# Kernel tuning notes

Hardware: AMD Instinct MI355X
Metric: run time of the kernel (lower is better)

## Reference

```python
import jax, jax.numpy as jnp
import numpy as np

B, S, D, U = 32, 2048, 512, 512

def setup_inputs() -> dict:
    key = jax.random.key(0)
    k1, k2, k3, k4, k5 = jax.random.split(key, 5)
    passage = jax.random.normal(k1, (B, S, D), dtype=jnp.float32)
    hidden = jax.random.normal(k2, (B, D), dtype=jnp.float32)
    mask = jnp.ones((B, S), dtype=jnp.float32)
    # learned params (Dense kernels, glorot-ish scale)
    W1 = jax.random.normal(k3, (D, U), dtype=jnp.float32) / np.sqrt(D)
    W2 = jax.random.normal(k4, (D, U), dtype=jnp.float32) / np.sqrt(D)
    Vw = jax.random.normal(k5, (U, 1), dtype=jnp.float32) / np.sqrt(U)
    Vb = jnp.zeros((1,), dtype=jnp.float32)
    return {"passage": passage, "hidden": hidden, "mask": mask,
            "W1": W1, "W2": W2, "Vw": Vw, "Vb": Vb}

def reference(passage, hidden, mask, W1, W2, Vw, Vb):
    # passage: [B,S,D], hidden: [B,D], mask: [B,S]
    h_proj = jnp.einsum('bd,du->bu', hidden, W2)[:, None, :]        # [B,1,U]
    p_proj = jnp.einsum('bsd,du->bsu', passage, W1)                  # [B,S,U]
    score = jnp.einsum('bsu,uo->bso', jnp.tanh(p_proj + h_proj), Vw) + Vb  # [B,S,1]
    score = score + ((1.0 - mask) * -1e30)[:, :, None]
    attention_weights = jax.nn.softmax(score, axis=1)                # [B,S,1]
    context_vector = jnp.sum(attention_weights * passage, axis=1)    # [B,D]
    return context_vector, attention_weights
```

## Files before the change

### kernel.cpp

```cpp
#include <hip/hip_runtime.h>
#include <hip/hip_bf16.h>
#include <cstddef>


#define NB 32
#define NS 2048
#define ND 512
#define NU 512

typedef __bf16 bf16_t;
typedef __bf16 bf16x8 __attribute__((ext_vector_type(8)));
typedef float floatx4 __attribute__((ext_vector_type(4)));

__global__ __launch_bounds__(256) void prep_kernel(
    const float* __restrict__ W1, bf16_t* __restrict__ W1p,
    const float* __restrict__ hidden, const float* __restrict__ W2,
    float* __restrict__ hproj) {
    if (blockIdx.x < 128) {
        int wave = threadIdx.x >> 6, lane = threadIdx.x & 63;
        int f = (blockIdx.x << 2) + wave;
        int kc = f >> 5, ng = f & 31;
        int q = lane >> 4, c = lane & 15;
        const float* src = W1 + (kc * 32 + q * 8) * 512 + ng * 16 + c;
        bf16x8 w;
#pragma unroll
        for (int jj = 0; jj < 8; ++jj) w[jj] = (bf16_t)src[jj * 512];
        ((bf16x8*)W1p)[(f << 6) + lane] = w;
    } else {
        __shared__ float h[ND];
        __shared__ float part[256];
        int bi = blockIdx.x - 128;
        int b = bi >> 2, ug = bi & 3;
        int t = threadIdx.x;
        h[t] = hidden[b * ND + t];
        h[t + 256] = hidden[b * ND + t + 256];
        __syncthreads();
        int u = (ug << 7) + (t & 127);
        int d0 = (t >> 7) << 8;
        float acc = 0.f;
#pragma unroll 8
        for (int d = d0; d < d0 + 256; ++d) acc = fmaf(h[d], W2[d * NU + u], acc);
        part[t] = acc;
        __syncthreads();
        if (t < 128) hproj[b * NU + u] = part[t] + part[t + 128];
    }
}

__global__ __launch_bounds__(512, 4) void score_kernel(
    const float* __restrict__ passage, const bf16_t* __restrict__ W1p,
    const float* __restrict__ hproj, const float* __restrict__ Vw,
    const float* __restrict__ Vb, float* __restrict__ scores) {
    __shared__ bf16_t Asf[64 * 512];
    const int tid = threadIdx.x;
    const int wave = tid >> 6, lane = tid & 63;
    const int q = lane >> 4, c = lane & 15;
    const int m0 = blockIdx.x * 64;
    const int b = m0 >> 11;
    const int ng0 = wave << 2;
    const bf16x8* Wq = (const bf16x8*)W1p;

#define LOAD_B(dst, kc_) {                                                   \
    _Pragma("unroll")                                                        \
    for (int j = 0; j < 4; ++j)                                              \
        dst[j] = Wq[((((kc_) << 5) + ng0 + j) << 6) + lane]; }

    bf16x8 b0[4], b1[4];
    LOAD_B(b0, 0);
    LOAD_B(b1, 1);

#pragma unroll
    for (int it = 0; it < 8; ++it) {
        int idx = it * 512 + tid;
        int row = idx >> 6, c8 = idx & 63;
        const float4* src = (const float4*)(passage + ((size_t)(m0 + row) << 9)) + (c8 << 1);
        float4 v0 = src[0], v1 = src[1];
        bf16x8 w;
        w[0] = (bf16_t)v0.x; w[1] = (bf16_t)v0.y; w[2] = (bf16_t)v0.z; w[3] = (bf16_t)v0.w;
        w[4] = (bf16_t)v1.x; w[5] = (bf16_t)v1.y; w[6] = (bf16_t)v1.z; w[7] = (bf16_t)v1.w;
        ((bf16x8*)(Asf + (row << 9)))[c8 ^ (row & 7)] = w;
    }
    __syncthreads();

    floatx4 acc[4][4];
#pragma unroll
    for (int i = 0; i < 4; ++i)
#pragma unroll
        for (int j = 0; j < 4; ++j) { floatx4 z = {0.f, 0.f, 0.f, 0.f}; acc[i][j] = z; }

#pragma unroll
    for (int kc = 0; kc < 16; ++kc) {
        bf16x8 bn[4];
        if (kc < 14) LOAD_B(bn, kc + 2);
        bf16x8 a[4];
        int chunk = (kc << 2) + q;
#pragma unroll
        for (int i = 0; i < 4; ++i)
            a[i] = ((const bf16x8*)(Asf + ((i * 16 + c) << 9)))[chunk ^ (c & 7)];
#pragma unroll
        for (int j = 0; j < 4; ++j)
#pragma unroll
            for (int i = 0; i < 4; ++i)
                acc[i][j] = __builtin_amdgcn_mfma_f32_16x16x32_bf16(a[i], b0[j], acc[i][j], 0, 0, 0);
#pragma unroll
        for (int j = 0; j < 4; ++j) { b0[j] = b1[j]; b1[j] = bn[j]; }
    }
#undef LOAD_B

    float sp[4][4];
#pragma unroll
    for (int i = 0; i < 4; ++i)
#pragma unroll
        for (int r = 0; r < 4; ++r) sp[i][r] = 0.f;
#pragma unroll
    for (int j = 0; j < 4; ++j) {
        int n = (wave << 6) + (j << 4) + c;
        float hp = hproj[(b << 9) + n];
        float vw = Vw[n];
#pragma unroll
        for (int i = 0; i < 4; ++i)
#pragma unroll
            for (int r = 0; r < 4; ++r) {
                float x = acc[i][j][r] + hp;
                float e = __expf(2.0f * x);
                float t = 1.0f - 2.0f * __builtin_amdgcn_rcpf(e + 1.0f);
                sp[i][r] = fmaf(t, vw, sp[i][r]);
            }
    }
#pragma unroll
    for (int off = 1; off < 16; off <<= 1)
#pragma unroll
        for (int i = 0; i < 4; ++i)
#pragma unroll
            for (int r = 0; r < 4; ++r)
                sp[i][r] += __shfl_xor(sp[i][r], off, 64);

    __syncthreads();
    float* red = (float*)Asf;
    if (c == 0) {
#pragma unroll
        for (int i = 0; i < 4; ++i)
#pragma unroll
            for (int r = 0; r < 4; ++r)
                red[wave * 64 + i * 16 + q * 4 + r] = sp[i][r];
    }
    __syncthreads();
    if (tid < 64) {
        float s = Vb[0];
#pragma unroll
        for (int w = 0; w < 8; ++w) s += red[w * 64 + tid];
        scores[m0 + tid] = s;
    }
}

__global__ __launch_bounds__(1024) void softmax_kernel(
    const float* __restrict__ mask, float* __restrict__ attn) {
    __shared__ float smx[16], ssm[16];
    int b = blockIdx.x, tid = threadIdx.x;
    int wave = tid >> 6, lane = tid & 63;
    const int base = b * NS;
    float v0 = attn[base + tid] + (1.0f - mask[base + tid]) * (-1e30f);
    float v1 = attn[base + 1024 + tid] + (1.0f - mask[base + 1024 + tid]) * (-1e30f);
    float mx = fmaxf(v0, v1);
#pragma unroll
    for (int off = 1; off < 64; off <<= 1) mx = fmaxf(mx, __shfl_xor(mx, off, 64));
    if (lane == 0) smx[wave] = mx;
    __syncthreads();
    mx = smx[0];
#pragma unroll
    for (int w = 1; w < 16; ++w) mx = fmaxf(mx, smx[w]);
    v0 = __expf(v0 - mx); v1 = __expf(v1 - mx);
    float sum = v0 + v1;
#pragma unroll
    for (int off = 1; off < 64; off <<= 1) sum += __shfl_xor(sum, off, 64);
    if (lane == 0) ssm[wave] = sum;
    __syncthreads();
    sum = 0.f;
#pragma unroll
    for (int w = 0; w < 16; ++w) sum += ssm[w];
    float inv = 1.0f / sum;
    attn[base + tid] = v0 * inv;
    attn[base + 1024 + tid] = v1 * inv;
}

__global__ __launch_bounds__(512) void context_kernel(
    const float* __restrict__ passage, const float* __restrict__ attn,
    float* __restrict__ ctx) {
    __shared__ float4 part[512];
    int bb = blockIdx.x >> 5, sc = blockIdx.x & 31, t = threadIdx.x;
    int col = t & 127, qh = t >> 7;
    const float4* p = (const float4*)(passage + (((size_t)bb * NS + sc * 64 + qh * 16) << 9));
    const float* wp = attn + bb * NS + sc * 64 + qh * 16;
    float ax = 0.f, ay = 0.f, az = 0.f, aw = 0.f;
#pragma unroll 16
    for (int s = 0; s < 16; ++s) {
        float w = wp[s];
        float4 v = p[(size_t)s * 128 + col];
        ax = fmaf(w, v.x, ax); ay = fmaf(w, v.y, ay);
        az = fmaf(w, v.z, az); aw = fmaf(w, v.w, aw);
    }
    float4 mine; mine.x = ax; mine.y = ay; mine.z = az; mine.w = aw;
    part[t] = mine;
    __syncthreads();
    if (t < 128) {
        float4 o1 = part[t + 128], o2 = part[t + 256], o3 = part[t + 384];
        float* dst = ctx + bb * ND + t * 4;
        atomicAdd(dst + 0, ax + o1.x + o2.x + o3.x);
        atomicAdd(dst + 1, ay + o1.y + o2.y + o3.y);
        atomicAdd(dst + 2, az + o1.z + o2.z + o3.z);
        atomicAdd(dst + 3, aw + o1.w + o2.w + o3.w);
    }
}

extern "C" void kernel_launch(void* const* d_in, const int* in_sizes, int n_in,
                              void* d_out, int out_size, void* d_ws, size_t ws_size,
                              hipStream_t stream) {
    const float* passage = (const float*)d_in[0];
    const float* hidden  = (const float*)d_in[1];
    const float* mask    = (const float*)d_in[2];
    const float* W1      = (const float*)d_in[3];
    const float* W2      = (const float*)d_in[4];
    const float* Vw      = (const float*)d_in[5];
    const float* Vb      = (const float*)d_in[6];

    float* ctx  = (float*)d_out;
    float* attn = (float*)d_out + NB * ND;

    bf16_t* W1p  = (bf16_t*)d_ws;
    float* hproj = (float*)((char*)d_ws + (size_t)NU * ND * 2);

    hipMemsetAsync(ctx, 0, (size_t)NB * ND * sizeof(float), stream);
    prep_kernel<<<dim3(256), dim3(256), 0, stream>>>(W1, W1p, hidden, W2, hproj);
    score_kernel<<<dim3(NB * NS / 64), dim3(512), 0, stream>>>(passage, W1p, hproj, Vw, Vb, attn);
    softmax_kernel<<<dim3(NB), dim3(1024), 0, stream>>>(mask, attn);
    context_kernel<<<dim3(NB * 32), dim3(512), 0, stream>>>(passage, attn, ctx);
}
```

Baseline: 288.2 us.

## Stream passage K-chunks via double-buffered global_load_lds in score kernel

Replaces the up-front load of the whole 64x512 passage tile (converted to bf16 in LDS) with a double-buffered ring of fp32 32-column chunks. The chunks are fetched by direct global-to-LDS DMA and converted to bf16 at fragment-load time. Blocks shrink to 4 waves that each cover 128 output columns with a 4x8 accumulator tile, and B fragments are loaded from global memory each step with no register prefetch. The aim is to overlap passage streaming with MFMA work and cut LDS footprint, at the cost of a barrier per K-step, more register pressure, and exposed W1p load latency.

Result: faster. 269.0 us (-6.7%).

```diff
diff --git a/kernel.cpp b/kernel.cpp
--- a/kernel.cpp
+++ b/kernel.cpp
@@ -11,6 +11,12 @@
 typedef __bf16 bf16_t;
 typedef __bf16 bf16x8 __attribute__((ext_vector_type(8)));
 typedef float floatx4 __attribute__((ext_vector_type(4)));
+
+__device__ __forceinline__ void dma16(const void* g, void* l) {
+    __builtin_amdgcn_global_load_lds(
+        (const __attribute__((address_space(1))) unsigned int*)g,
+        (__attribute__((address_space(3))) unsigned int*)l, 16, 0, 0);
+}
 
 __global__ __launch_bounds__(256) void prep_kernel(
     const float* __restrict__ W1, bf16_t* __restrict__ W1p,
@@ -46,65 +52,71 @@
     }
 }
 
-__global__ __launch_bounds__(512, 4) void score_kernel(
+__global__ __launch_bounds__(256, 2) void score_kernel(
     const float* __restrict__ passage, const bf16_t* __restrict__ W1p,
     const float* __restrict__ hproj, const float* __restrict__ Vw,
     const float* __restrict__ Vb, float* __restrict__ scores) {
-    __shared__ bf16_t Asf[64 * 512];
+    __shared__ float ring[2 * 64 * 32];
+    __shared__ float red[4 * 64];
     const int tid = threadIdx.x;
     const int wave = tid >> 6, lane = tid & 63;
     const int q = lane >> 4, c = lane & 15;
     const int m0 = blockIdx.x * 64;
     const int b = m0 >> 11;
-    const int ng0 = wave << 2;
+    const int ng0 = wave << 3;
     const bf16x8* Wq = (const bf16x8*)W1p;
 
-#define LOAD_B(dst, kc_) {                                                   \
-    _Pragma("unroll")                                                        \
-    for (int j = 0; j < 4; ++j)                                              \
-        dst[j] = Wq[((((kc_) << 5) + ng0 + j) << 6) + lane]; }
-
-    bf16x8 b0[4], b1[4];
-    LOAD_B(b0, 0);
-    LOAD_B(b1, 1);
-
-#pragma unroll
-    for (int it = 0; it < 8; ++it) {
-        int idx = it * 512 + tid;
-        int row = idx >> 6, c8 = idx & 63;
-        const float4* src = (const float4*)(passage + ((size_t)(m0 + row) << 9)) + (c8 << 1);
-        float4 v0 = src[0], v1 = src[1];
-        bf16x8 w;
-        w[0] = (bf16_t)v0.x; w[1] = (bf16_t)v0.y; w[2] = (bf16_t)v0.z; w[3] = (bf16_t)v0.w;
-        w[4] = (bf16_t)v1.x; w[5] = (bf16_t)v1.y; w[6] = (bf16_t)v1.z; w[7] = (bf16_t)v1.w;
-        ((bf16x8*)(Asf + (row << 9)))[c8 ^ (row & 7)] = w;
-    }
-    __syncthreads();
-
-    floatx4 acc[4][4];
+    const int ch0 = wave * 2;
+    const int r0 = ch0 * 8 + (lane >> 3);
+    const int k0 = ((lane & 7) - r0) & 7;
+    const int r1 = r0 + 8;
+    const int k1 = ((lane & 7) - r1) & 7;
+    const float* g0 = passage + (size_t)(m0 + r0) * ND + k0 * 4;
+    const float* g1 = passage + (size_t)(m0 + r1) * ND + k1 * 4;
+    char* l0a = (char*)ring + ch0 * 1024;
+    char* l1a = (char*)ring + ch0 * 1024 + 1024;
+    char* l0b = (char*)ring + 8192 + ch0 * 1024;
+    char* l1b = (char*)ring + 8192 + ch0 * 1024 + 1024;
+
+    dma16(g0, l0a);
+    dma16(g1, l1a);
+    __syncthreads();
+
+    floatx4 acc[4][8];
 #pragma unroll
     for (int i = 0; i < 4; ++i)
 #pragma unroll
-        for (int j = 0; j < 4; ++j) { floatx4 z = {0.f, 0.f, 0.f, 0.f}; acc[i][j] = z; }
-
-#pragma unroll
+        for (int j = 0; j < 8; ++j) { floatx4 z = {0.f, 0.f, 0.f, 0.f}; acc[i][j] = z; }
+
     for (int kc = 0; kc < 16; ++kc) {
-        bf16x8 bn[4];
-        if (kc < 14) LOAD_B(bn, kc + 2);
-        bf16x8 a[4];
-        int chunk = (kc << 2) + q;
-#pragma unroll
-        for (int i = 0; i < 4; ++i)
-            a[i] = ((const bf16x8*)(Asf + ((i * 16 + c) << 9)))[chunk ^ (c & 7)];
-#pragma unroll
-        for (int j = 0; j < 4; ++j)
-#pragma unroll
-            for (int i = 0; i < 4; ++i)
-                acc[i][j] = __builtin_amdgcn_mfma_f32_16x16x32_bf16(a[i], b0[j], acc[i][j], 0, 0, 0);
-#pragma unroll
-        for (int j = 0; j < 4; ++j) { b0[j] = b1[j]; b1[j] = bn[j]; }
-    }
-#undef LOAD_B
+        if (kc < 15) {
+            const float* ga = g0 + (kc + 1) * 32;
+            const float* gb = g1 + (kc + 1) * 32;
+            if ((kc + 1) & 1) { dma16(ga, l0b); dma16(gb, l1b); }
+            else              { dma16(ga, l0a); dma16(gb, l1a); }
+        }
+        bf16x8 bb[8];
+#pragma unroll
+        for (int j = 0; j < 8; ++j)
+            bb[j] = Wq[(((kc << 5) + ng0 + j) << 6) + lane];
+        const float* sl = ring + (kc & 1) * 2048;
+#pragma unroll
+        for (int i = 0; i < 4; ++i) {
+            int r = i * 16 + c;
+            const float* rp = sl + r * 32;
+            floatx4 lo = *(const floatx4*)(rp + (((q << 1) + r) & 7) * 4);
+            floatx4 hi = *(const floatx4*)(rp + (((q << 1) + 1 + r) & 7) * 4);
+            bf16x8 a;
+            a[0] = (bf16_t)lo[0]; a[1] = (bf16_t)lo[1];
+            a[2] = (bf16_t)lo[2]; a[3] = (bf16_t)lo[3];
+            a[4] = (bf16_t)hi[0]; a[5] = (bf16_t)hi[1];
+            a[6] = (bf16_t)hi[2]; a[7] = (bf16_t)hi[3];
+#pragma unroll
+            for (int j = 0; j < 8; ++j)
+                acc[i][j] = __builtin_amdgcn_mfma_f32_16x16x32_bf16(a, bb[j], acc[i][j], 0, 0, 0);
+        }
+        __syncthreads();
+    }
 
     float sp[4][4];
 #pragma unroll
@@ -112,8 +124,8 @@
 #pragma unroll
         for (int r = 0; r < 4; ++r) sp[i][r] = 0.f;
 #pragma unroll
-    for (int j = 0; j < 4; ++j) {
-        int n = (wave << 6) + (j << 4) + c;
+    for (int j = 0; j < 8; ++j) {
+        int n = (wave << 7) + (j << 4) + c;
         float hp = hproj[(b << 9) + n];
         float vw = Vw[n];
 #pragma unroll
@@ -134,8 +146,6 @@
             for (int r = 0; r < 4; ++r)
                 sp[i][r] += __shfl_xor(sp[i][r], off, 64);
 
-    __syncthreads();
-    float* red = (float*)Asf;
     if (c == 0) {
 #pragma unroll
         for (int i = 0; i < 4; ++i)
@@ -144,12 +154,8 @@
                 red[wave * 64 + i * 16 + q * 4 + r] = sp[i][r];
     }
     __syncthreads();
-    if (tid < 64) {
-        float s = Vb[0];
-#pragma unroll
-        for (int w = 0; w < 8; ++w) s += red[w * 64 + tid];
-        scores[m0 + tid] = s;
-    }
+    if (tid < 64)
+        scores[m0 + tid] = red[tid] + red[64 + tid] + red[128 + tid] + red[192 + tid] + Vb[0];
 }
 
 __global__ __launch_bounds__(1024) void softmax_kernel(
@@ -230,7 +236,7 @@
 
     hipMemsetAsync(ctx, 0, (size_t)NB * ND * sizeof(float), stream);
     prep_kernel<<<dim3(256), dim3(256), 0, stream>>>(W1, W1p, hidden, W2, hproj);
-    score_kernel<<<dim3(NB * NS / 64), dim3(512), 0, stream>>>(passage, W1p, hproj, Vw, Vb, attn);
+    score_kernel<<<dim3(NB * NS / 64), dim3(256), 0, stream>>>(passage, W1p, hproj, Vw, Vb, attn);
     softmax_kernel<<<dim3(NB), dim3(1024), 0, stream>>>(mask, attn);
     context_kernel<<<dim3(NB * 32), dim3(512), 0, stream>>>(passage, attn, ctx);
 }
```
